# Kernel tuning notes

Hardware: AMD Instinct MI355X
Metric: run time of the kernel (lower is better)

Reference implementation:

```python
import jax, jax.numpy as jnp
import numpy as np

B, T, D = 2, 2048, 1024
H = 16
HD = D // H  # head_dim = 64 (kv_rank == embed_dim)
INT4_MIN, INT4_MAX = -8.0, 7.0


def _int4_quant_dequant(x):
    # per-token amax over last dim (head_dim), as in INT4Quantizer with 4-D input
    amax = jnp.max(jnp.abs(x), axis=-1, keepdims=True)
    amax = jnp.maximum(amax, 1e-5)
    scale = amax / 7.0
    q = jnp.clip(jnp.round(x / scale), INT4_MIN, INT4_MAX)  # stored as int8 in cache
    return q * scale


def setup_inputs() -> dict:
    key = jax.random.key(0)
    ks = jax.random.split(key, 11)
    s = 1.0 / np.sqrt(D)
    return {
        "query": jax.random.normal(ks[0], (B, T, D), jnp.float32),
        "key": jax.random.normal(ks[1], (B, T, D), jnp.float32),
        "value": jax.random.normal(ks[2], (B, T, D), jnp.float32),
        "Wq": jax.random.normal(ks[3], (D, D), jnp.float32) * s,
        "bq": jnp.zeros((D,), jnp.float32),
        "Wk": jax.random.normal(ks[4], (D, D), jnp.float32) * s,
        "bk": jnp.zeros((D,), jnp.float32),
        "Wv": jax.random.normal(ks[5], (D, D), jnp.float32) * s,
        "bv": jnp.zeros((D,), jnp.float32),
        "Wo": jax.random.normal(ks[6], (D, D), jnp.float32) * s,
        "bo": jnp.zeros((D,), jnp.float32),
    }


def reference(query, key, value, Wq, bq, Wk, bk, Wv, bv, Wo, bo):
    # projections (nn.Linear: x @ W.T + b)
    q = query @ Wq.T + bq
    k = key @ Wk.T + bk
    v = value @ Wv.T + bv
    # (B, T, D) -> (B, H, T, HD)
    q = q.reshape(B, T, H, HD).transpose(0, 2, 1, 3)
    k = k.reshape(B, T, H, HD).transpose(0, 2, 1, 3)
    v = v.reshape(B, T, H, HD).transpose(0, 2, 1, 3)
    # INT4 quantized KV cache update (use_cache=True): quantize -> scatter into
    # fresh cache -> dequantize the just-written block == quant/dequant of k, v
    k = _int4_quant_dequant(k)
    v = _int4_quant_dequant(v)
    # attention
    scale = HD ** (-0.5)
    attn = jnp.einsum("bhqd,bhkd->bhqk", q, k) * scale
    attn = jax.nn.softmax(attn.astype(jnp.float32), axis=-1).astype(query.dtype)
    out = jnp.einsum("bhqk,bhkd->bhqd", attn, v)
    out = out.transpose(0, 2, 1, 3).reshape(B, T, D)
    out = out @ Wo.T + bo
    return out
```

## Files before the change

kernel.cpp:

```cpp
#include <hip/hip_runtime.h>

typedef unsigned short u16;
typedef unsigned int u32;
typedef float f32x4 __attribute__((ext_vector_type(4)));
typedef short s16x8 __attribute__((ext_vector_type(8)));
typedef u16 u16x8 __attribute__((ext_vector_type(8)));
typedef u16 u16x4 __attribute__((ext_vector_type(4)));
typedef _Float16 h16x8 __attribute__((ext_vector_type(8)));

#define B_ 2
#define T_ 2048
#define H_ 16
#define D_ 1024
#define HD_ 64
#define NTOK (B_*T_)

__device__ __forceinline__ u16 f2b(float f){
  u32 u = __float_as_uint(f);
  return (u16)((u + 0x7fffu + ((u>>16)&1u)) >> 16);
}
__device__ __forceinline__ float b2f(u16 h){ return __uint_as_float(((u32)h)<<16); }

__device__ __forceinline__ void gload_lds16(const u16* g, u16* s){
  __builtin_amdgcn_global_load_lds((const __attribute__((address_space(1))) void*)g,
                                   (__attribute__((address_space(3))) void*)s, 16, 0, 0);
}

template<int ROWS, int WAVES>
__device__ __forceinline__ void stage_tile(const u16* __restrict__ g, size_t ldg,
                                           u16* s, int tid){
  const int w = tid>>6, l = tid&63;
  const int rw = ROWS/WAVES;
  #pragma unroll
  for (int i=0;i<ROWS/(WAVES*8);i++){
    int r0 = w*rw + i*8;
    int r  = r0 + (l>>3);
    int u  = (l&7) ^ (r&7);
    gload_lds16(g + (size_t)r*ldg + (size_t)u*8, s + r0*64);
  }
}

__device__ __forceinline__ u16x8 read_frag(const u16* s, int r, int kk, int l){
  int u = (kk<<2) | (l>>4);
  int phys = u ^ (r&7);
  return *(const u16x8*)(s + r*64 + phys*8);
}

__device__ __forceinline__ void stage_tile32(const u16* __restrict__ g, size_t ldg,
                                             u16* s, int tid){
  const int w = tid>>6, l = tid&63;
  int r0 = w*16;
  int r  = r0 + (l>>2);
  int v  = (l&3) ^ ((r>>1)&3);
  gload_lds16(g + (size_t)r*ldg + (size_t)v*8, s + r0*32);
}
__device__ __forceinline__ u16x8 read_frag32(const u16* s, int r, int l){
  int phys = (l>>4) ^ ((r>>1)&3);
  return *(const u16x8*)(s + r*32 + phys*8);
}

__device__ __forceinline__ f32x4 mfma_bf16(u16x8 a, u16x8 b, f32x4 c){
  return __builtin_amdgcn_mfma_f32_16x16x32_bf16(
      __builtin_bit_cast(s16x8,a), __builtin_bit_cast(s16x8,b), c, 0,0,0);
}
__device__ __forceinline__ f32x4 mfma_f16(u16x8 a, u16x8 b, f32x4 c){
  return __builtin_amdgcn_mfma_f32_16x16x32_f16(
      __builtin_bit_cast(h16x8,a), __builtin_bit_cast(h16x8,b), c, 0,0,0);
}

__device__ __forceinline__ void split_bf4(const float* in, u16* hi, u16* lo, int i){
  f32x4 v = ((const f32x4*)in)[i];
  u16x4 h, lw;
  #pragma unroll
  for (int j=0;j<4;j++){
    u16 hb = f2b(v[j]);
    h[j] = hb;
    lw[j] = f2b(v[j] - b2f(hb));
  }
  ((u16x4*)hi)[i] = h;
  ((u16x4*)lo)[i] = lw;
}
__device__ __forceinline__ void split_h4(const float* in, u16* out, int i){
  f32x4 v = ((const f32x4*)in)[i];
  u16x4 o;
  #pragma unroll
  for (int j=0;j<4;j++){
    _Float16 t = (_Float16)v[j];
    o[j] = __builtin_bit_cast(u16, t);
  }
  ((u16x4*)out)[i] = o;
}

__global__ void split_inputs_kernel(const float* __restrict__ q, const float* __restrict__ k,
                                    const float* __restrict__ v,
                                    u16* __restrict__ qh, u16* __restrict__ khi, u16* __restrict__ klo,
                                    u16* __restrict__ vhi, u16* __restrict__ vlo){
  int i = blockIdx.x*256 + threadIdx.x;
  int which = blockIdx.y;
  if (which==0)      split_h4 (q, qh, i);
  else if (which==1) split_bf4(k, khi, klo, i);
  else               split_bf4(v, vhi, vlo, i);
}

__global__ void split_weights_kernel(const float* __restrict__ wq, const float* __restrict__ wk,
                                     const float* __restrict__ wv, const float* __restrict__ wo,
                                     u16* __restrict__ wqh, u16* __restrict__ wkh, u16* __restrict__ wkl,
                                     u16* __restrict__ wvh, u16* __restrict__ wvl, u16* __restrict__ woh){
  int i = blockIdx.x*256 + threadIdx.x;
  int which = blockIdx.y;
  if (which==0)      split_h4 (wq, wqh, i);
  else if (which==1) split_bf4(wk, wkh, wkl, i);
  else if (which==2) split_bf4(wv, wvh, wvl, i);
  else               split_h4 (wo, woh, i);
}

template<int F16OUT>
__global__ __launch_bounds__(512)
void gemm1(const u16* __restrict__ Ah, const u16* __restrict__ Wh,
           const float* __restrict__ bias, void* __restrict__ Cout)
{
  __shared__ u16 sA[2][128*64];
  __shared__ u16 sW[2][64*64];
  const int tid = threadIdx.x, l = tid&63, w = tid>>6, l15 = l&15, g = l>>4;
  const int wm = w>>1, wn = w&1;
  const int bm = blockIdx.x, bn = blockIdx.y;
  const u16* A0 = Ah + (size_t)bm*128*D_;
  const u16* W0 = Wh + (size_t)bn*64*D_;
  f32x4 acc[2][2] = {};

  stage_tile<128,8>(A0, D_, sA[0], tid);
  stage_tile<64 ,8>(W0, D_, sW[0], tid);
  __syncthreads();
  for (int t=0; t<D_/64; ++t){
    const int cur = t&1;
    if (t+1 < D_/64){
      stage_tile<128,8>(A0 + (t+1)*64, D_, sA[cur^1], tid);
      stage_tile<64 ,8>(W0 + (t+1)*64, D_, sW[cur^1], tid);
    }
    #pragma unroll
    for (int kk=0;kk<2;kk++){
      u16x8 af[2], wf[2];
      #pragma unroll
      for (int fm=0;fm<2;fm++) af[fm] = read_frag(sA[cur], wm*32+fm*16+l15, kk, l);
      #pragma unroll
      for (int fn=0;fn<2;fn++) wf[fn] = read_frag(sW[cur], wn*32+fn*16+l15, kk, l);
      #pragma unroll
      for (int fm=0;fm<2;fm++)
        #pragma unroll
        for (int fn=0;fn<2;fn++)
          acc[fm][fn] = mfma_f16(af[fm], wf[fn], acc[fm][fn]);
    }
    __syncthreads();
  }

  #pragma unroll
  for (int fn=0; fn<2; fn++){
    int col = bn*64 + wn*32 + fn*16 + l15;
    float bv = bias[col];
    #pragma unroll
    for (int fm=0; fm<2; fm++){
      int r0 = bm*128 + wm*32 + fm*16 + g*4;
      #pragma unroll
      for (int j=0;j<4;j++){
        float v = acc[fm][fn][j] + bv;
        if constexpr (F16OUT){
          ((_Float16*)Cout)[(size_t)(r0+j)*D_ + col] = (_Float16)v;
        } else {
          ((float*)Cout)[(size_t)(r0+j)*D_ + col] = v;
        }
      }
    }
  }
}

template<int QMODE>
__global__ __launch_bounds__(512)
void gemm3_quant(const u16* __restrict__ Ah, const u16* __restrict__ Al,
                 const u16* __restrict__ Wh, const u16* __restrict__ Wl,
                 const float* __restrict__ bias, u16* __restrict__ Out)
{
  extern __shared__ u16 sm[];
  const int tid = threadIdx.x, l = tid&63, w = tid>>6, l15 = l&15, g = l>>4;
  const int wm = w>>1, wn = w&1;
  const int bm = blockIdx.x, bn = blockIdx.y;
  const u16* A0 = Ah + (size_t)bm*128*D_;
  const u16* A1 = Al + (size_t)bm*128*D_;
  const u16* W0 = Wh + (size_t)bn*128*D_;
  const u16* W1 = Wl + (size_t)bn*128*D_;
  constexpr int TS = 128*32;
  f32x4 acc[2][4] = {};

  auto stage = [&](int buf, int t){
    u16* base = sm + buf*4*TS;
    stage_tile32(A0 + t*32, D_, base       , tid);
    stage_tile32(A1 + t*32, D_, base +   TS, tid);
    stage_tile32(W0 + t*32, D_, base + 2*TS, tid);
    stage_tile32(W1 + t*32, D_, base + 3*TS, tid);
  };
  stage(0,0);
  __syncthreads();
  for (int t=0; t<D_/32; ++t){
    const int cur = t&1;
    if (t+1 < D_/32) stage(cur^1, t+1);
    const u16* base = sm + cur*4*TS;
    u16x8 ahh[2], ahl[2], whh[4], whl[4];
    #pragma unroll
    for (int fm=0;fm<2;fm++){
      ahh[fm] = read_frag32(base     , wm*32+fm*16+l15, l);
      ahl[fm] = read_frag32(base+  TS, wm*32+fm*16+l15, l);
    }
    #pragma unroll
    for (int fn=0;fn<4;fn++){
      whh[fn] = read_frag32(base+2*TS, wn*64+fn*16+l15, l);
      whl[fn] = read_frag32(base+3*TS, wn*64+fn*16+l15, l);
    }
    #pragma unroll
    for (int fm=0;fm<2;fm++)
      #pragma unroll
      for (int fn=0;fn<4;fn++){
        acc[fm][fn] = mfma_bf16(ahh[fm], whh[fn], acc[fm][fn]);
        acc[fm][fn] = mfma_bf16(ahh[fm], whl[fn], acc[fm][fn]);
        acc[fm][fn] = mfma_bf16(ahl[fm], whh[fn], acc[fm][fn]);
      }
    __syncthreads();
  }

  #pragma unroll
  for (int fn=0;fn<4;fn++){
    float bv = bias[bn*128 + wn*64 + fn*16 + l15];
    #pragma unroll
    for (int fm=0;fm<2;fm++)
      #pragma unroll
      for (int j=0;j<4;j++) acc[fm][fn][j] += bv;
  }

  u16 (*sdq)[136] = (u16(*)[136])sm;
  #pragma unroll
  for (int fm=0;fm<2;fm++)
    #pragma unroll
    for (int j=0;j<4;j++){
      float a = 0.f;
      #pragma unroll
      for (int fn=0;fn<4;fn++) a = fmaxf(a, fabsf(acc[fm][fn][j]));
      a = fmaxf(a, __shfl_xor(a,1)); a = fmaxf(a, __shfl_xor(a,2));
      a = fmaxf(a, __shfl_xor(a,4)); a = fmaxf(a, __shfl_xor(a,8));
      a = fmaxf(a, 1e-5f);
      float scale = a / 7.0f;
      int row = wm*32 + fm*16 + g*4 + j;
      #pragma unroll
      for (int fn=0;fn<4;fn++){
        float q = rintf(acc[fm][fn][j] / scale);
        q = fminf(fmaxf(q, -8.f), 7.f);
        _Float16 dq = (_Float16)(q * scale);
        int col = wn*64 + fn*16 + l15;
        if (QMODE==1) sdq[row][col] = __builtin_bit_cast(u16, dq);
        else          sdq[col][row] = __builtin_bit_cast(u16, dq);
      }
    }
  __syncthreads();

  if (QMODE==1){
    int r = tid>>2, seg = tid&3;
    u16* dst = Out + (size_t)(bm*128 + r)*D_ + bn*128 + seg*32;
    #pragma unroll
    for (int i=0;i<4;i++)
      *(u16x8*)(dst + i*8) = *(const u16x8*)&sdq[r][seg*32 + i*8];
  } else {
    int c = tid>>2, seg = tid&3;
    int h = 2*bn + (c>>6), d = c&63, b = bm>>4;
    u16* dst = Out + ((size_t)((b*H_+h)*HD_ + d))*T_ + (bm&15)*128 + seg*32;
    #pragma unroll
    for (int i=0;i<4;i++)
      *(u16x8*)(dst + i*8) = *(const u16x8*)&sdq[c][seg*32 + i*8];
  }
}

__global__ __launch_bounds__(256)
void attn_kernel(const _Float16* __restrict__ Qp, const u16* __restrict__ Kdq,
                 const u16* __restrict__ Vt, _Float16* __restrict__ Aout)
{
  __shared__ u16 sK[2][64*64];
  __shared__ u16 sV[2][64*64];
  __shared__ u16 sP[4][16*64];
  const int tid = threadIdx.x, l = tid&63, w = tid>>6;
  const int d = blockIdx.x;
  const int xcd = d & 7, slot = d >> 3;
  const int bh = xcd*4 + (slot>>5);
  const int qb = slot & 31;
  const int b = bh>>4, h = bh&15;

  u16x8 qf[2];
  {
    int qr = qb*64 + w*16 + (l&15);
    const _Float16* qrow = Qp + (size_t)(b*T_+qr)*D_ + h*HD_;
    #pragma unroll
    for (int kk=0;kk<2;kk++){
      int d0 = kk*32 + ((l>>4)<<3);
      h16x8 qv = *(const h16x8*)(qrow + d0);
      qv = qv * (_Float16)0.125f;
      qf[kk] = __builtin_bit_cast(u16x8, qv);
    }
  }

  f32x4 o[4] = {};
  float lsp[4] = {0.f,0.f,0.f,0.f};

  const u16* Kb = Kdq + (size_t)(b*T_)*D_ + h*HD_;
  const u16* Vb = Vt  + (size_t)((b*H_+h)*HD_)*T_;

  stage_tile<64,4>(Kb, D_, sK[0], tid);
  stage_tile<64,4>(Vb, T_, sV[0], tid);
  __syncthreads();

  for (int kt=0; kt<T_/64; kt++){
    const int cur = kt&1;
    if (kt+1 < T_/64){
      stage_tile<64,4>(Kb + (size_t)((kt+1)*64)*D_, D_, sK[cur^1], tid);
      stage_tile<64,4>(Vb + (kt+1)*64,              T_, sV[cur^1], tid);
    }

    u16x8 kf[4][2];
    #pragma unroll
    for (int fn=0;fn<4;fn++)
      #pragma unroll
      for (int kk=0;kk<2;kk++) kf[fn][kk] = read_frag(sK[cur], fn*16+(l&15), kk, l);

    f32x4 s[4] = {};
    #pragma unroll
    for (int fn=0;fn<4;fn++)
      #pragma unroll
      for (int kk=0;kk<2;kk++) s[fn] = mfma_f16(qf[kk], kf[fn][kk], s[fn]);

    #pragma unroll
    for (int fn=0;fn<4;fn++)
      #pragma unroll
      for (int j=0;j<4;j++){
        float p = __expf(s[fn][j]);
        lsp[j] += p;
        int r = ((l>>4)<<2) + j;
        int c = fn*16 + (l&15);
        int phys = (c>>3) ^ (r&7);
        _Float16 ph = (_Float16)p;
        sP[w][r*64 + phys*8 + (c&7)] = __builtin_bit_cast(u16, ph);
      }

    u16x8 vf[4][2], pf[2];
    #pragma unroll
    for (int fn=0;fn<4;fn++)
      #pragma unroll
      for (int kk=0;kk<2;kk++) vf[fn][kk] = read_frag(sV[cur], fn*16+(l&15), kk, l);
    #pragma unroll
    for (int kk=0;kk<2;kk++) pf[kk] = read_frag(sP[w], (l&15), kk, l);
    #pragma unroll
    for (int fn=0;fn<4;fn++)
      #pragma unroll
      for (int kk=0;kk<2;kk++) o[fn] = mfma_f16(pf[kk], vf[fn][kk], o[fn]);

    __syncthreads();
  }

  #pragma unroll
  for (int j=0;j<4;j++){
    float t = lsp[j];
    t += __shfl_xor(t,1); t += __shfl_xor(t,2);
    t += __shfl_xor(t,4); t += __shfl_xor(t,8);
    lsp[j] = t;
  }

  #pragma unroll
  for (int fn=0;fn<4;fn++)
    #pragma unroll
    for (int j=0;j<4;j++){
      int qr  = qb*64 + w*16 + ((l>>4)<<2) + j;
      int col = h*HD_ + fn*16 + (l&15);
      Aout[(size_t)(b*T_+qr)*D_ + col] = (_Float16)(o[fn][j] / lsp[j]);
    }
}

extern "C" void kernel_launch(void* const* d_in, const int* in_sizes, int n_in,
                              void* d_out, int out_size, void* d_ws, size_t ws_size,
                              hipStream_t stream)
{
  (void)in_sizes; (void)n_in; (void)out_size; (void)ws_size;
  const float* query = (const float*)d_in[0];
  const float* key   = (const float*)d_in[1];
  const float* value = (const float*)d_in[2];
  const float* Wq = (const float*)d_in[3];
  const float* bq = (const float*)d_in[4];
  const float* Wk = (const float*)d_in[5];
  const float* bk = (const float*)d_in[6];
  const float* Wv = (const float*)d_in[7];
  const float* bv = (const float*)d_in[8];
  const float* Wo = (const float*)d_in[9];
  const float* bo = (const float*)d_in[10];
  float* out = (float*)d_out;

  char* p = (char*)d_ws;
  auto take = [&](size_t n){ char* r = p; p += (n + 255) & ~(size_t)255; return r; };
  const size_t big = (size_t)NTOK*D_*2;
  const size_t wsz = (size_t)D_*D_*2;

  u16* q_h  = (u16*)take(big);
  u16* khi  = (u16*)take(big);  u16* klo = (u16*)take(big);
  u16* vhi  = (u16*)take(big);  u16* vlo = (u16*)take(big);
  u16* wq_h = (u16*)take(wsz);
  u16* wkh  = (u16*)take(wsz);  u16* wkl = (u16*)take(wsz);
  u16* wvh  = (u16*)take(wsz);  u16* wvl = (u16*)take(wsz);
  u16* wo_h = (u16*)take(wsz);
  u16*  Qp  = (u16*)take(big);
  u16*  Kdq = (u16*)take(big);
  u16*  Vtp = (u16*)take(big);
  u16*  Ao  = (u16*)take(big);

  split_inputs_kernel <<<dim3(NTOK*D_/4/256, 3), 256, 0, stream>>>(
      query, key, value, q_h, khi, klo, vhi, vlo);
  split_weights_kernel<<<dim3(D_*D_/4/256, 4), 256, 0, stream>>>(
      Wq, Wk, Wv, Wo, wq_h, wkh, wkl, wvh, wvl, wo_h);

  gemm1<1><<<dim3(32,16), 512, 0, stream>>>(q_h, wq_h, bq, Qp);
  gemm3_quant<1><<<dim3(32,8), 512, 64*1024, stream>>>(khi, klo, wkh, wkl, bk, Kdq);
  gemm3_quant<2><<<dim3(32,8), 512, 64*1024, stream>>>(vhi, vlo, wvh, wvl, bv, Vtp);

  attn_kernel<<<1024, 256, 0, stream>>>((const _Float16*)Qp, Kdq, Vtp, (_Float16*)Ao);

  gemm1<0><<<dim3(32,16), 512, 0, stream>>>(Ao, wo_h, bo, out);
}
```

Measured before the change: 192.2 us.

## Rewrite attention with 32x32 MFMA, register-resident P and exp2 softmax

The attention kernel moves from 16x16x32 to 32x32x16 MFMA tiles and computes S transposed so the probabilities stay in registers. A lane shuffle re-forms them into the A operand instead of going through LDS. The softmax scale and log2(e) are folded into the Q projection epilogue so exp2 can be used directly. Row sums are accumulated with packed fdot2, and each block now handles 128 query rows, so the grid is halved. This removes the LDS round trip for P and improves MFMA efficiency, at the cost of more register pressure and fewer blocks in flight.

```diff
diff --git a/kernel.cpp b/kernel.cpp
--- a/kernel.cpp
+++ b/kernel.cpp
@@ -3,10 +3,13 @@
 typedef unsigned short u16;
 typedef unsigned int u32;
 typedef float f32x4 __attribute__((ext_vector_type(4)));
+typedef float f32x16 __attribute__((ext_vector_type(16)));
 typedef short s16x8 __attribute__((ext_vector_type(8)));
 typedef u16 u16x8 __attribute__((ext_vector_type(8)));
 typedef u16 u16x4 __attribute__((ext_vector_type(4)));
+typedef u32 u32x4 __attribute__((ext_vector_type(4)));
 typedef _Float16 h16x8 __attribute__((ext_vector_type(8)));
+typedef _Float16 h16x2 __attribute__((ext_vector_type(2)));
 
 #define B_ 2
 #define T_ 2048
@@ -15,6 +18,8 @@
 #define HD_ 64
 #define NTOK (B_*T_)
 
+#define QSCALE 0.18033688011112042f
+
 __device__ __forceinline__ u16 f2b(float f){
   u32 u = __float_as_uint(f);
   return (u16)((u + 0x7fffu + ((u>>16)&1u)) >> 16);
@@ -43,6 +48,10 @@
 __device__ __forceinline__ u16x8 read_frag(const u16* s, int r, int kk, int l){
   int u = (kk<<2) | (l>>4);
   int phys = u ^ (r&7);
+  return *(const u16x8*)(s + r*64 + phys*8);
+}
+__device__ __forceinline__ u16x8 rfragT(const u16* s, int r, int ks, int hi){
+  int phys = (ks*2 + hi) ^ (r&7);
   return *(const u16x8*)(s + r*64 + phys*8);
 }
 
@@ -59,13 +68,39 @@
   return *(const u16x8*)(s + r*32 + phys*8);
 }
 
-__device__ __forceinline__ f32x4 mfma_bf16(u16x8 a, u16x8 b, f32x4 c){
+__device__ __forceinline__ f32x4 mfma16_f16(u16x8 a, u16x8 b, f32x4 c){
+  return __builtin_amdgcn_mfma_f32_16x16x32_f16(
+      __builtin_bit_cast(h16x8,a), __builtin_bit_cast(h16x8,b), c, 0,0,0);
+}
+__device__ __forceinline__ f32x4 mfma16_bf16(u16x8 a, u16x8 b, f32x4 c){
   return __builtin_amdgcn_mfma_f32_16x16x32_bf16(
       __builtin_bit_cast(s16x8,a), __builtin_bit_cast(s16x8,b), c, 0,0,0);
 }
-__device__ __forceinline__ f32x4 mfma_f16(u16x8 a, u16x8 b, f32x4 c){
-  return __builtin_amdgcn_mfma_f32_16x16x32_f16(
+__device__ __forceinline__ f32x16 mfma32_f16(u16x8 a, u16x8 b, f32x16 c){
+  return __builtin_amdgcn_mfma_f32_32x32x16_f16(
       __builtin_bit_cast(h16x8,a), __builtin_bit_cast(h16x8,b), c, 0,0,0);
+}
+
+__device__ __forceinline__ float ex2(float x){
+#if __has_builtin(__builtin_amdgcn_exp2f)
+  return __builtin_amdgcn_exp2f(x);
+#else
+  return exp2f(x);
+#endif
+}
+__device__ __forceinline__ u32 pk2(float a, float b){
+  u16 x = __builtin_bit_cast(u16, (_Float16)a);
+  u16 y = __builtin_bit_cast(u16, (_Float16)b);
+  return (u32)x | ((u32)y<<16);
+}
+__device__ __forceinline__ float dot2acc(u32 wv, float c){
+#if __has_builtin(__builtin_amdgcn_fdot2)
+  h16x2 one2 = {(_Float16)1.0f, (_Float16)1.0f};
+  return __builtin_amdgcn_fdot2(__builtin_bit_cast(h16x2, wv), one2, c, false);
+#else
+  h16x2 v = __builtin_bit_cast(h16x2, wv);
+  return c + (float)v[0] + (float)v[1];
+#endif
 }
 
 __device__ __forceinline__ void split_bf4(const float* in, u16* hi, u16* lo, int i){
@@ -117,11 +152,11 @@
 template<int F16OUT>
 __global__ __launch_bounds__(512)
 void gemm1(const u16* __restrict__ Ah, const u16* __restrict__ Wh,
-           const float* __restrict__ bias, void* __restrict__ Cout)
+           const float* __restrict__ bias, void* __restrict__ Cout, float oscale)
 {
   __shared__ u16 sA[2][128*64];
   __shared__ u16 sW[2][64*64];
-  const int tid = threadIdx.x, l = tid&63, w = tid>>6, l15 = l&15, g = l>>4;
+  const int tid = threadIdx.x, l = tid&63, l15 = l&15, g = l>>4, w = tid>>6;
   const int wm = w>>1, wn = w&1;
   const int bm = blockIdx.x, bn = blockIdx.y;
   const u16* A0 = Ah + (size_t)bm*128*D_;
@@ -148,7 +183,7 @@
       for (int fm=0;fm<2;fm++)
         #pragma unroll
         for (int fn=0;fn<2;fn++)
-          acc[fm][fn] = mfma_f16(af[fm], wf[fn], acc[fm][fn]);
+          acc[fm][fn] = mfma16_f16(af[fm], wf[fn], acc[fm][fn]);
     }
     __syncthreads();
   }
@@ -162,7 +197,7 @@
       int r0 = bm*128 + wm*32 + fm*16 + g*4;
       #pragma unroll
       for (int j=0;j<4;j++){
-        float v = acc[fm][fn][j] + bv;
+        float v = (acc[fm][fn][j] + bv) * oscale;
         if constexpr (F16OUT){
           ((_Float16*)Cout)[(size_t)(r0+j)*D_ + col] = (_Float16)v;
         } else {
@@ -218,9 +253,9 @@
     for (int fm=0;fm<2;fm++)
       #pragma unroll
       for (int fn=0;fn<4;fn++){
-        acc[fm][fn] = mfma_bf16(ahh[fm], whh[fn], acc[fm][fn]);
-        acc[fm][fn] = mfma_bf16(ahh[fm], whl[fn], acc[fm][fn]);
-        acc[fm][fn] = mfma_bf16(ahl[fm], whh[fn], acc[fm][fn]);
+        acc[fm][fn] = mfma16_bf16(ahh[fm], whh[fn], acc[fm][fn]);
+        acc[fm][fn] = mfma16_bf16(ahh[fm], whl[fn], acc[fm][fn]);
+        acc[fm][fn] = mfma16_bf16(ahl[fm], whh[fn], acc[fm][fn]);
       }
     __syncthreads();
   }
@@ -266,12 +301,12 @@
     for (int i=0;i<4;i++)
       *(u16x8*)(dst + i*8) = *(const u16x8*)&sdq[r][seg*32 + i*8];
   } else {
-    int c = tid>>2, seg = tid&3;
-    int h = 2*bn + (c>>6), d = c&63, b = bm>>4;
-    u16* dst = Out + ((size_t)((b*H_+h)*HD_ + d))*T_ + (bm&15)*128 + seg*32;
+    int cc = tid>>2, seg = tid&3;
+    int hh = 2*bn + (cc>>6), dd = cc&63, b = bm>>4;
+    u16* dst = Out + ((size_t)((b*H_+hh)*HD_ + dd))*T_ + (bm&15)*128 + seg*32;
     #pragma unroll
     for (int i=0;i<4;i++)
-      *(u16x8*)(dst + i*8) = *(const u16x8*)&sdq[c][seg*32 + i*8];
+      *(u16x8*)(dst + i*8) = *(const u16x8*)&sdq[cc][seg*32 + i*8];
   }
 }
 
@@ -281,29 +316,24 @@
 {
   __shared__ u16 sK[2][64*64];
   __shared__ u16 sV[2][64*64];
-  __shared__ u16 sP[4][16*64];
-  const int tid = threadIdx.x, l = tid&63, w = tid>>6;
+  __shared__ float sRl[128];
+  const int tid = threadIdx.x, l = tid&63, c = l&31, hi = l>>5, w = tid>>6;
   const int d = blockIdx.x;
   const int xcd = d & 7, slot = d >> 3;
-  const int bh = xcd*4 + (slot>>5);
-  const int qb = slot & 31;
+  const int bh = xcd*4 + (slot>>4);
+  const int qb = slot & 15;
   const int b = bh>>4, h = bh&15;
 
-  u16x8 qf[2];
+  u16x8 qf[4];
   {
-    int qr = qb*64 + w*16 + (l&15);
-    const _Float16* qrow = Qp + (size_t)(b*T_+qr)*D_ + h*HD_;
-    #pragma unroll
-    for (int kk=0;kk<2;kk++){
-      int d0 = kk*32 + ((l>>4)<<3);
-      h16x8 qv = *(const h16x8*)(qrow + d0);
-      qv = qv * (_Float16)0.125f;
-      qf[kk] = __builtin_bit_cast(u16x8, qv);
-    }
-  }
-
-  f32x4 o[4] = {};
-  float lsp[4] = {0.f,0.f,0.f,0.f};
+    const u16* qrow = (const u16*)Qp + (size_t)(b*T_ + qb*128 + w*32 + c)*D_ + h*HD_;
+    #pragma unroll
+    for (int ks=0;ks<4;ks++)
+      qf[ks] = *(const u16x8*)(qrow + ks*16 + hi*8);
+  }
+
+  f32x16 o0 = {}, o1 = {};
+  float lsp = 0.f;
 
   const u16* Kb = Kdq + (size_t)(b*T_)*D_ + h*HD_;
   const u16* Vb = Vt  + (size_t)((b*H_+h)*HD_)*T_;
@@ -319,62 +349,62 @@
       stage_tile<64,4>(Vb + (kt+1)*64,              T_, sV[cur^1], tid);
     }
 
-    u16x8 kf[4][2];
-    #pragma unroll
-    for (int fn=0;fn<4;fn++)
-      #pragma unroll
-      for (int kk=0;kk<2;kk++) kf[fn][kk] = read_frag(sK[cur], fn*16+(l&15), kk, l);
-
-    f32x4 s[4] = {};
-    #pragma unroll
-    for (int fn=0;fn<4;fn++)
-      #pragma unroll
-      for (int kk=0;kk<2;kk++) s[fn] = mfma_f16(qf[kk], kf[fn][kk], s[fn]);
-
-    #pragma unroll
-    for (int fn=0;fn<4;fn++)
-      #pragma unroll
-      for (int j=0;j<4;j++){
-        float p = __expf(s[fn][j]);
-        lsp[j] += p;
-        int r = ((l>>4)<<2) + j;
-        int c = fn*16 + (l&15);
-        int phys = (c>>3) ^ (r&7);
-        _Float16 ph = (_Float16)p;
-        sP[w][r*64 + phys*8 + (c&7)] = __builtin_bit_cast(u16, ph);
+    u16x8 vf0[4], vf1[4];
+    #pragma unroll
+    for (int ks=0;ks<4;ks++){
+      vf0[ks] = rfragT(sV[cur],      c, ks, hi);
+      vf1[ks] = rfragT(sV[cur], 32 + c, ks, hi);
+    }
+
+    #pragma unroll
+    for (int kb=0;kb<2;kb++){
+      f32x16 s = {};
+      #pragma unroll
+      for (int ks=0;ks<4;ks++){
+        u16x8 kf = rfragT(sK[cur], kb*32 + c, ks, hi);
+        s = mfma32_f16(kf, qf[ks], s);
       }
-
-    u16x8 vf[4][2], pf[2];
-    #pragma unroll
-    for (int fn=0;fn<4;fn++)
-      #pragma unroll
-      for (int kk=0;kk<2;kk++) vf[fn][kk] = read_frag(sV[cur], fn*16+(l&15), kk, l);
-    #pragma unroll
-    for (int kk=0;kk<2;kk++) pf[kk] = read_frag(sP[w], (l&15), kk, l);
-    #pragma unroll
-    for (int fn=0;fn<4;fn++)
-      #pragma unroll
-      for (int kk=0;kk<2;kk++) o[fn] = mfma_f16(pf[kk], vf[fn][kk], o[fn]);
-
+      float p[16];
+      #pragma unroll
+      for (int r=0;r<16;r++) p[r] = ex2(s[r]);
+      u32 x0 = pk2(p[0],p[1]),   x1 = pk2(p[2],p[3]);
+      u32 x2 = pk2(p[4],p[5]),   x3 = pk2(p[6],p[7]);
+      u32 x4 = pk2(p[8],p[9]),   x5 = pk2(p[10],p[11]);
+      u32 x6 = pk2(p[12],p[13]), x7 = pk2(p[14],p[15]);
+      lsp = dot2acc(x0,lsp); lsp = dot2acc(x1,lsp);
+      lsp = dot2acc(x2,lsp); lsp = dot2acc(x3,lsp);
+      lsp = dot2acc(x4,lsp); lsp = dot2acc(x5,lsp);
+      lsp = dot2acc(x6,lsp); lsp = dot2acc(x7,lsp);
+      u32 y0 = __shfl_xor(x0,32), y1 = __shfl_xor(x1,32);
+      u32 y2 = __shfl_xor(x2,32), y3 = __shfl_xor(x3,32);
+      u32 y4 = __shfl_xor(x4,32), y5 = __shfl_xor(x5,32);
+      u32 y6 = __shfl_xor(x6,32), y7 = __shfl_xor(x7,32);
+      const bool hb = (hi != 0);
+      u32x4 pw0 = { hb ? y2 : x0, hb ? y3 : x1, hb ? x2 : y0, hb ? x3 : y1 };
+      u32x4 pw1 = { hb ? y6 : x4, hb ? y7 : x5, hb ? x6 : y4, hb ? x7 : y5 };
+      u16x8 pa0 = __builtin_bit_cast(u16x8, pw0);
+      u16x8 pa1 = __builtin_bit_cast(u16x8, pw1);
+      o0 = mfma32_f16(pa0, vf0[kb*2+0], o0);
+      o1 = mfma32_f16(pa0, vf1[kb*2+0], o1);
+      o0 = mfma32_f16(pa1, vf0[kb*2+1], o0);
+      o1 = mfma32_f16(pa1, vf1[kb*2+1], o1);
+    }
     __syncthreads();
   }
 
-  #pragma unroll
-  for (int j=0;j<4;j++){
-    float t = lsp[j];
-    t += __shfl_xor(t,1); t += __shfl_xor(t,2);
-    t += __shfl_xor(t,4); t += __shfl_xor(t,8);
-    lsp[j] = t;
-  }
-
-  #pragma unroll
-  for (int fn=0;fn<4;fn++)
-    #pragma unroll
-    for (int j=0;j<4;j++){
-      int qr  = qb*64 + w*16 + ((l>>4)<<2) + j;
-      int col = h*HD_ + fn*16 + (l&15);
-      Aout[(size_t)(b*T_+qr)*D_ + col] = (_Float16)(o[fn][j] / lsp[j]);
-    }
+  float lt = lsp + __shfl_xor(lsp, 32);
+  if (l < 32) sRl[w*32 + c] = 1.0f / lt;
+  __syncthreads();
+
+  #pragma unroll
+  for (int r=0;r<16;r++){
+    int crow = (r&3) + 8*(r>>2) + 4*hi;
+    float rl = sRl[w*32 + crow];
+    int qr = qb*128 + w*32 + crow;
+    _Float16* arow = Aout + (size_t)(b*T_+qr)*D_ + h*HD_;
+    arow[c]      = (_Float16)(o0[r]*rl);
+    arow[32 + c] = (_Float16)(o1[r]*rl);
+  }
 }
 
 extern "C" void kernel_launch(void* const* d_in, const int* in_sizes, int n_in,
@@ -417,11 +447,11 @@
   split_weights_kernel<<<dim3(D_*D_/4/256, 4), 256, 0, stream>>>(
       Wq, Wk, Wv, Wo, wq_h, wkh, wkl, wvh, wvl, wo_h);
 
-  gemm1<1><<<dim3(32,16), 512, 0, stream>>>(q_h, wq_h, bq, Qp);
+  gemm1<1><<<dim3(32,16), 512, 0, stream>>>(q_h, wq_h, bq, Qp, QSCALE);
   gemm3_quant<1><<<dim3(32,8), 512, 64*1024, stream>>>(khi, klo, wkh, wkl, bk, Kdq);
   gemm3_quant<2><<<dim3(32,8), 512, 64*1024, stream>>>(vhi, vlo, wvh, wvl, bv, Vtp);
 
-  attn_kernel<<<1024, 256, 0, stream>>>((const _Float16*)Qp, Kdq, Vtp, (_Float16*)Ao);
-
-  gemm1<0><<<dim3(32,16), 512, 0, stream>>>(Ao, wo_h, bo, out);
-}
+  attn_kernel<<<512, 256, 0, stream>>>((const _Float16*)Qp, Kdq, Vtp, (_Float16*)Ao);
+
+  gemm1<0><<<dim3(32,16), 512, 0, stream>>>(Ao, wo_h, bo, out, 1.0f);
+}
```

Result: faster. 182.3 us (-5.1%).
